# Kernel tuning notes

Measured on AMD Instinct MI355X. Metric: run time of the kernel, lower is better.

## Reference

```python
import jax, jax.numpy as jnp
import numpy as np

N_NODES = 50000
IN_DIM = 256
LATENT = 128
HIDDEN = 2 * LATENT  # 256


def _xavier(key, fan_in, fan_out):
    # matches nn.init.xavier_uniform_ on a [out, in] weight; we store as [in, out]
    limit = float(np.sqrt(6.0 / (fan_in + fan_out)))
    return jax.random.uniform(key, (fan_in, fan_out), jnp.float32, -limit, limit)


def setup_inputs() -> dict:
    key = jax.random.key(0)
    ks = jax.random.split(key, 8)
    x = jax.random.normal(ks[0], (N_NODES, IN_DIM), jnp.float32)
    edge_index = jax.random.randint(ks[1], (2, 800000), 0, N_NODES, jnp.int64)
    W1 = _xavier(ks[2], IN_DIM, HIDDEN)
    b1 = jnp.zeros((HIDDEN,), jnp.float32)
    Wmu = _xavier(ks[3], HIDDEN, LATENT)
    bmu = jnp.zeros((LATENT,), jnp.float32)
    Wlv = _xavier(ks[4], HIDDEN, LATENT)
    blv = jnp.zeros((LATENT,), jnp.float32)
    return {"x": x, "edge_index": edge_index, "W1": W1, "b1": b1,
            "Wmu": Wmu, "bmu": bmu, "Wlv": Wlv, "blv": blv}


def _gcn_layer(x, W, b, src, dst):
    # PyG GCNConv: h = x @ W; add self loops; symmetric norm; scatter-add; + bias
    h = x @ W  # [N, out]
    ones = jnp.ones(src.shape[0], x.dtype)
    deg = jax.ops.segment_sum(ones, dst, num_segments=N_NODES) + 1.0  # +1 for self loop
    dinv = jax.lax.rsqrt(deg)  # deg >= 1 always
    norm = dinv[src] * dinv[dst]  # [E]
    agg = jax.ops.segment_sum(h[src] * norm[:, None], dst, num_segments=N_NODES)
    agg = agg + h * (dinv * dinv)[:, None]  # self-loop contribution, norm_ii = 1/deg_i
    return agg + b


def reference(x, edge_index, W1, b1, Wmu, bmu, Wlv, blv):
    src, dst = edge_index[0], edge_index[1]
    z = _gcn_layer(x, W1, b1, src, dst)
    z = jax.nn.relu(z)
    # dropout in eval mode == identity
    mu = _gcn_layer(z, Wmu, bmu, src, dst)
    logvar = _gcn_layer(z, Wlv, blv, src, dst)
    return (mu, logvar)
```

## Files before the change

kernel.cpp:

```cpp
#include <hip/hip_runtime.h>

#define N_NODES 50000
#define E_EDGES 800000
#define D 256
#define L 128
#define CAP 64

typedef __attribute__((ext_vector_type(8))) short bf16x8;
typedef __attribute__((ext_vector_type(4))) float f32x4;

__device__ __forceinline__ float bf2f(unsigned short u) {
    union { unsigned int i; float f; } v; v.i = ((unsigned int)u) << 16; return v.f;
}
__device__ __forceinline__ unsigned short f2bf(float f) {
    union { float f; unsigned int i; } v; v.f = f;
    unsigned int r = v.i + 0x7fffu + ((v.i >> 16) & 1u);
    return (unsigned short)(r >> 16);
}

__global__ __launch_bounds__(256) void zero_i(int* __restrict__ p, int n) {
    int i = blockIdx.x * 256 + threadIdx.x;
    if (i < n) p[i] = 0;
}

__global__ __launch_bounds__(256) void fill_fixed(const int* __restrict__ src,
                                                  const int* __restrict__ dst,
                                                  int* __restrict__ cursor,
                                                  int* __restrict__ bucket) {
    int e = blockIdx.x * 256 + threadIdx.x;
    if (e >= E_EDGES) return;
    int d = dst[e];
    int pos = atomicAdd(&cursor[d], 1);
    if (pos < CAP) bucket[d * CAP + pos] = src[e];
}

__global__ __launch_bounds__(256) void dinv_fin(const int* __restrict__ cursor,
                                                float* __restrict__ dinv) {
    int i = blockIdx.x * 256 + threadIdx.x;
    if (i < N_NODES) dinv[i] = rsqrtf((float)cursor[i] + 1.0f);
}

__global__ __launch_bounds__(256) void prep_w(
    const float* __restrict__ W1, const float* __restrict__ Wmu,
    const float* __restrict__ Wlv, const float* __restrict__ bmu,
    const float* __restrict__ blv,
    unsigned short* __restrict__ W1h, unsigned short* __restrict__ W1l,
    unsigned short* __restrict__ Wch, unsigned short* __restrict__ Wcl,
    float* __restrict__ bcat) {
    int b = blockIdx.x, t = threadIdx.x;
    if (b < 256) {
        int n = b, k = t;
        float w = W1[k * 256 + n];
        unsigned short h = f2bf(w);
        W1h[n * 256 + k] = h;
        W1l[n * 256 + k] = f2bf(w - bf2f(h));
    } else {
        int n = b - 256, k = t;
        float w = (n < 128) ? Wmu[k * 128 + n] : Wlv[k * 128 + (n - 128)];
        unsigned short h = f2bf(w);
        Wch[n * 256 + k] = h;
        Wcl[n * 256 + k] = f2bf(w - bf2f(h));
        if (b == 256) bcat[t] = (t < 128) ? bmu[t] : blv[t - 128];
    }
}

__global__ __launch_bounds__(256, 3) void gemm_mfma(
    const float* __restrict__ A,
    const unsigned short* __restrict__ Bth, const unsigned short* __restrict__ Btl,
    unsigned short* __restrict__ Hout, int M)
{
    __shared__ unsigned short Bsh[256 * 32];
    __shared__ unsigned short Bsl[256 * 32];
    const int t = threadIdx.x;
    const int lane = t & 63, wave = t >> 6;
    const int row0 = blockIdx.x * 64 + wave * 16;
    const int m_ = lane & 15, q = lane >> 4;
    int rA = row0 + m_; if (rA >= M) rA = M - 1;
    const float* Ap = A + (size_t)rA * 256;
    const int bn = t >> 2;
    const int bc = t & 3;

    f32x4 acc[16];
    const f32x4 zf = {0.f, 0.f, 0.f, 0.f};
#pragma unroll
    for (int nt = 0; nt < 16; ++nt) acc[nt] = zf;

    for (int ks = 0; ks < 8; ++ks) {
        const int k0 = ks * 32;
        bf16x8 gbh[4], gbl[4];
#pragma unroll
        for (int i = 0; i < 4; ++i) {
            int n = bn + i * 64;
            gbh[i] = *(const bf16x8*)(Bth + n * 256 + k0 + bc * 8);
            gbl[i] = *(const bf16x8*)(Btl + n * 256 + k0 + bc * 8);
        }
        float4 av0 = *(const float4*)(Ap + k0 + q * 8);
        float4 av1 = *(const float4*)(Ap + k0 + q * 8 + 4);
        __syncthreads();
#pragma unroll
        for (int i = 0; i < 4; ++i) {
            int n = bn + i * 64;
            int cc = (bc ^ ((n >> 1) & 3)) * 8;
            *(bf16x8*)&Bsh[n * 32 + cc] = gbh[i];
            *(bf16x8*)&Bsl[n * 32 + cc] = gbl[i];
        }
        float af[8] = {av0.x, av0.y, av0.z, av0.w, av1.x, av1.y, av1.z, av1.w};
        bf16x8 ah, al;
#pragma unroll
        for (int j = 0; j < 8; ++j) {
            unsigned short h = f2bf(af[j]);
            ah[j] = (short)h;
            al[j] = (short)f2bf(af[j] - bf2f(h));
        }
        __syncthreads();
#pragma unroll
        for (int nt = 0; nt < 16; ++nt) {
            int n = nt * 16 + m_;
            int cr = (q ^ ((n >> 1) & 3)) * 8;
            bf16x8 bh = *(const bf16x8*)&Bsh[n * 32 + cr];
            bf16x8 bl = *(const bf16x8*)&Bsl[n * 32 + cr];
            acc[nt] = __builtin_amdgcn_mfma_f32_16x16x32_bf16(ah, bh, acc[nt], 0, 0, 0);
            acc[nt] = __builtin_amdgcn_mfma_f32_16x16x32_bf16(ah, bl, acc[nt], 0, 0, 0);
            acc[nt] = __builtin_amdgcn_mfma_f32_16x16x32_bf16(al, bh, acc[nt], 0, 0, 0);
        }
    }
    int rbase = row0 + q * 4;
#pragma unroll
    for (int r = 0; r < 4; ++r) {
        int grow = rbase + r;
        if (grow >= M) continue;
#pragma unroll
        for (int nt = 0; nt < 16; ++nt) {
            int gcol = nt * 16 + m_;
            Hout[(size_t)grow * 256 + gcol] = f2bf(acc[nt][r]);
        }
    }
}

__global__ __launch_bounds__(256, 3) void gemm_bf16(
    const unsigned short* __restrict__ A,
    const unsigned short* __restrict__ Bth, const unsigned short* __restrict__ Btl,
    unsigned short* __restrict__ Tout, int M)
{
    __shared__ unsigned short Bsh[256 * 32];
    __shared__ unsigned short Bsl[256 * 32];
    const int t = threadIdx.x;
    const int lane = t & 63, wave = t >> 6;
    const int row0 = blockIdx.x * 64 + wave * 16;
    const int m_ = lane & 15, q = lane >> 4;
    int rA = row0 + m_; if (rA >= M) rA = M - 1;
    const unsigned short* Ap = A + (size_t)rA * 256;
    const int bn = t >> 2;
    const int bc = t & 3;

    f32x4 acc[16];
    const f32x4 zf = {0.f, 0.f, 0.f, 0.f};
#pragma unroll
    for (int nt = 0; nt < 16; ++nt) acc[nt] = zf;

    for (int ks = 0; ks < 8; ++ks) {
        const int k0 = ks * 32;
        bf16x8 gbh[4], gbl[4];
#pragma unroll
        for (int i = 0; i < 4; ++i) {
            int n = bn + i * 64;
            gbh[i] = *(const bf16x8*)(Bth + n * 256 + k0 + bc * 8);
            gbl[i] = *(const bf16x8*)(Btl + n * 256 + k0 + bc * 8);
        }
        bf16x8 ah = *(const bf16x8*)(Ap + k0 + q * 8);
        __syncthreads();
#pragma unroll
        for (int i = 0; i < 4; ++i) {
            int n = bn + i * 64;
            int cc = (bc ^ ((n >> 1) & 3)) * 8;
            *(bf16x8*)&Bsh[n * 32 + cc] = gbh[i];
            *(bf16x8*)&Bsl[n * 32 + cc] = gbl[i];
        }
        __syncthreads();
#pragma unroll
        for (int nt = 0; nt < 16; ++nt) {
            int n = nt * 16 + m_;
            int cr = (q ^ ((n >> 1) & 3)) * 8;
            bf16x8 bh = *(const bf16x8*)&Bsh[n * 32 + cr];
            bf16x8 bl = *(const bf16x8*)&Bsl[n * 32 + cr];
            acc[nt] = __builtin_amdgcn_mfma_f32_16x16x32_bf16(ah, bh, acc[nt], 0, 0, 0);
            acc[nt] = __builtin_amdgcn_mfma_f32_16x16x32_bf16(ah, bl, acc[nt], 0, 0, 0);
        }
    }
    int rbase = row0 + q * 4;
#pragma unroll
    for (int r = 0; r < 4; ++r) {
        int grow = rbase + r;
        if (grow >= M) continue;
#pragma unroll
        for (int nt = 0; nt < 16; ++nt) {
            int gcol = nt * 16 + m_;
            Tout[(size_t)grow * 256 + gcol] = f2bf(acc[nt][r]);
        }
    }
}

__global__ __launch_bounds__(256) void gather_pre(
    const unsigned short* __restrict__ Hs,
    const int* __restrict__ bucket, const int* __restrict__ cnt_,
    const float* __restrict__ dinv, const float* __restrict__ bias,
    unsigned short* __restrict__ OutZ,
    float* __restrict__ mu, float* __restrict__ lv, int mode)
{
    const int lane = threadIdx.x & 63;
    const int hl = lane & 31;
    const int bb = lane & 32;
    const int node = blockIdx.x * 8 + (threadIdx.x >> 5);
    const int col = hl * 8;
    int cnt = cnt_[node]; if (cnt > CAP) cnt = CAP;
    float dn = dinv[node];

    int   s0r = 0, s1r = 0;
    float w0r = 0.f, w1r = 0.f;
    if (hl < cnt)      { s0r = bucket[node * CAP + hl];      w0r = dinv[s0r] * dn; }
    if (hl + 32 < cnt) { s1r = bucket[node * CAP + 32 + hl]; w1r = dinv[s1r] * dn; }

    float sl = dn * dn;
    bf16x8 hv = *(const bf16x8*)(Hs + (size_t)node * D + col);
    float a[8];
#pragma unroll
    for (int p = 0; p < 8; ++p) a[p] = bf2f((unsigned short)hv[p]) * sl;

    const int cnt0 = cnt < 32 ? cnt : 32;
    int j = 0;
    for (; j + 3 < cnt0; j += 4) {
        int t0 = __shfl(s0r, bb + j,     64), t1 = __shfl(s0r, bb + j + 1, 64);
        int t2 = __shfl(s0r, bb + j + 2, 64), t3 = __shfl(s0r, bb + j + 3, 64);
        float w0 = __shfl(w0r, bb + j,     64), w1 = __shfl(w0r, bb + j + 1, 64);
        float w2 = __shfl(w0r, bb + j + 2, 64), w3 = __shfl(w0r, bb + j + 3, 64);
        bf16x8 u0 = *(const bf16x8*)(Hs + (size_t)t0 * D + col);
        bf16x8 u1 = *(const bf16x8*)(Hs + (size_t)t1 * D + col);
        bf16x8 u2 = *(const bf16x8*)(Hs + (size_t)t2 * D + col);
        bf16x8 u3 = *(const bf16x8*)(Hs + (size_t)t3 * D + col);
#pragma unroll
        for (int p = 0; p < 8; ++p) a[p] = fmaf(bf2f((unsigned short)u0[p]), w0, a[p]);
#pragma unroll
        for (int p = 0; p < 8; ++p) a[p] = fmaf(bf2f((unsigned short)u1[p]), w1, a[p]);
#pragma unroll
        for (int p = 0; p < 8; ++p) a[p] = fmaf(bf2f((unsigned short)u2[p]), w2, a[p]);
#pragma unroll
        for (int p = 0; p < 8; ++p) a[p] = fmaf(bf2f((unsigned short)u3[p]), w3, a[p]);
    }
    for (; j < cnt0; ++j) {
        int   t0 = __shfl(s0r, bb + j, 64);
        float w0 = __shfl(w0r, bb + j, 64);
        bf16x8 u0 = *(const bf16x8*)(Hs + (size_t)t0 * D + col);
#pragma unroll
        for (int p = 0; p < 8; ++p) a[p] = fmaf(bf2f((unsigned short)u0[p]), w0, a[p]);
    }
    if (cnt > 32) {
        for (int j2 = 0; j2 < cnt - 32; ++j2) {
            int   t0 = __shfl(s1r, bb + j2, 64);
            float w0 = __shfl(w1r, bb + j2, 64);
            bf16x8 u0 = *(const bf16x8*)(Hs + (size_t)t0 * D + col);
#pragma unroll
            for (int p = 0; p < 8; ++p) a[p] = fmaf(bf2f((unsigned short)u0[p]), w0, a[p]);
        }
    }

    float4 b0 = *(const float4*)(bias + col);
    float4 b1 = *(const float4*)(bias + col + 4);
    float bf[8] = {b0.x, b0.y, b0.z, b0.w, b1.x, b1.y, b1.z, b1.w};
    if (mode == 0) {
        bf16x8 o;
#pragma unroll
        for (int p = 0; p < 8; ++p) o[p] = (short)f2bf(fmaxf(a[p] + bf[p], 0.f));
        *(bf16x8*)(OutZ + (size_t)node * D + col) = o;
    } else {
        float4 o0, o1;
        o0.x = a[0] + bf[0]; o0.y = a[1] + bf[1];
        o0.z = a[2] + bf[2]; o0.w = a[3] + bf[3];
        o1.x = a[4] + bf[4]; o1.y = a[5] + bf[5];
        o1.z = a[6] + bf[6]; o1.w = a[7] + bf[7];
        float* Op = (col < 128) ? (mu + (size_t)node * L + col)
                                : (lv + (size_t)node * L + (col - 128));
        *(float4*)Op = o0;
        *(float4*)(Op + 4) = o1;
    }
}

extern "C" void kernel_launch(void* const* d_in, const int* in_sizes, int n_in,
                              void* d_out, int out_size, void* d_ws, size_t ws_size,
                              hipStream_t stream) {
    const float* x   = (const float*)d_in[0];
    const int*   ei  = (const int*)d_in[1];
    const float* W1  = (const float*)d_in[2];
    const float* b1  = (const float*)d_in[3];
    const float* Wmu = (const float*)d_in[4];
    const float* bmu = (const float*)d_in[5];
    const float* Wlv = (const float*)d_in[6];
    const float* blv = (const float*)d_in[7];
    const int* src = ei;
    const int* dst = ei + E_EDGES;

    const size_t NF = (size_t)N_NODES * D;
    unsigned short* Hb = (unsigned short*)d_ws;
    unsigned short* Z  = Hb + NF;
    unsigned short* T  = Z + NF;
    unsigned short* W1h = T + NF;
    unsigned short* W1l = W1h + 65536;
    unsigned short* Wch = W1l + 65536;
    unsigned short* Wcl = Wch + 65536;
    float* bcat = (float*)(Wcl + 65536);
    float* dinv = bcat + 256;
    int* cursor = (int*)(dinv + N_NODES);
    int* bucket = cursor + N_NODES;
    float* mu = (float*)d_out;
    float* lv = mu + (size_t)N_NODES * L;

    zero_i<<<(N_NODES + 255) / 256, 256, 0, stream>>>(cursor, N_NODES);
    fill_fixed<<<(E_EDGES + 255) / 256, 256, 0, stream>>>(src, dst, cursor, bucket);
    dinv_fin<<<(N_NODES + 255) / 256, 256, 0, stream>>>(cursor, dinv);

    prep_w<<<512, 256, 0, stream>>>(W1, Wmu, Wlv, bmu, blv, W1h, W1l, Wch, Wcl, bcat);

    const int gemm_blocks = (N_NODES + 63) / 64;
    const int gat_blocks  = N_NODES / 8;
    gemm_mfma<<<gemm_blocks, 256, 0, stream>>>(x, W1h, W1l, Hb, N_NODES);
    gather_pre<<<gat_blocks, 256, 0, stream>>>(Hb, bucket, cursor, dinv, b1,
                                               Z, nullptr, nullptr, 0);
    gemm_bf16<<<gemm_blocks, 256, 0, stream>>>(Z, Wch, Wcl, T, N_NODES);
    gather_pre<<<gat_blocks, 256, 0, stream>>>(T, bucket, cursor, dinv, bcat,
                                               nullptr, mu, lv, 1);
}
```

Before: 336.2 us.

## Retile GEMMs to 128-row blocks with 2x2 wave grid and shared A tiles

Both dense GEMM kernels move from 64-row blocks, where each wave owns 16 rows and all 256 columns, to 128-row blocks split over a 2x2 grid of waves (64 rows by 128 columns each). A is staged through swizzled LDS, and each wave reuses every B fragment across four row subtiles. This cuts LDS traffic for B per MFMA and halves the number of blocks, at the cost of more accumulator registers and a lower occupancy bound (2 blocks per CU instead of 3). The cursor zeroing is also folded into the weight-prep kernel, removing one launch.

```diff
diff --git a/kernel.cpp b/kernel.cpp
--- a/kernel.cpp
+++ b/kernel.cpp
@@ -16,11 +16,6 @@
     union { float f; unsigned int i; } v; v.f = f;
     unsigned int r = v.i + 0x7fffu + ((v.i >> 16) & 1u);
     return (unsigned short)(r >> 16);
-}
-
-__global__ __launch_bounds__(256) void zero_i(int* __restrict__ p, int n) {
-    int i = blockIdx.x * 256 + threadIdx.x;
-    if (i < n) p[i] = 0;
 }
 
 __global__ __launch_bounds__(256) void fill_fixed(const int* __restrict__ src,
@@ -40,13 +35,13 @@
     if (i < N_NODES) dinv[i] = rsqrtf((float)cursor[i] + 1.0f);
 }
 
-__global__ __launch_bounds__(256) void prep_w(
+__global__ __launch_bounds__(256) void setup(
     const float* __restrict__ W1, const float* __restrict__ Wmu,
     const float* __restrict__ Wlv, const float* __restrict__ bmu,
     const float* __restrict__ blv,
     unsigned short* __restrict__ W1h, unsigned short* __restrict__ W1l,
     unsigned short* __restrict__ Wch, unsigned short* __restrict__ Wcl,
-    float* __restrict__ bcat) {
+    float* __restrict__ bcat, int* __restrict__ cursor) {
     int b = blockIdx.x, t = threadIdx.x;
     if (b < 256) {
         int n = b, k = t;
@@ -54,148 +49,208 @@
         unsigned short h = f2bf(w);
         W1h[n * 256 + k] = h;
         W1l[n * 256 + k] = f2bf(w - bf2f(h));
-    } else {
+    } else if (b < 512) {
         int n = b - 256, k = t;
         float w = (n < 128) ? Wmu[k * 128 + n] : Wlv[k * 128 + (n - 128)];
         unsigned short h = f2bf(w);
         Wch[n * 256 + k] = h;
         Wcl[n * 256 + k] = f2bf(w - bf2f(h));
         if (b == 256) bcat[t] = (t < 128) ? bmu[t] : blv[t - 128];
-    }
-}
-
-__global__ __launch_bounds__(256, 3) void gemm_mfma(
+    } else {
+        int i = (b - 512) * 256 + t;
+        if (i < N_NODES) cursor[i] = 0;
+    }
+}
+
+__global__ __launch_bounds__(256, 2) void gemm_mfma(
     const float* __restrict__ A,
     const unsigned short* __restrict__ Bth, const unsigned short* __restrict__ Btl,
     unsigned short* __restrict__ Hout, int M)
 {
+    __shared__ unsigned short Ash[128 * 32];
+    __shared__ unsigned short Asl[128 * 32];
     __shared__ unsigned short Bsh[256 * 32];
     __shared__ unsigned short Bsl[256 * 32];
     const int t = threadIdx.x;
     const int lane = t & 63, wave = t >> 6;
-    const int row0 = blockIdx.x * 64 + wave * 16;
     const int m_ = lane & 15, q = lane >> 4;
-    int rA = row0 + m_; if (rA >= M) rA = M - 1;
-    const float* Ap = A + (size_t)rA * 256;
-    const int bn = t >> 2;
-    const int bc = t & 3;
-
-    f32x4 acc[16];
+    const int wr = wave >> 1, wc = wave & 1;
+    const int row0 = blockIdx.x * 128;
+    const int sr = t >> 2;
+    const int sc = t & 3;
+
+    f32x4 acc[4][8];
     const f32x4 zf = {0.f, 0.f, 0.f, 0.f};
 #pragma unroll
-    for (int nt = 0; nt < 16; ++nt) acc[nt] = zf;
+    for (int rs = 0; rs < 4; ++rs)
+#pragma unroll
+        for (int nt = 0; nt < 8; ++nt) acc[rs][nt] = zf;
 
     for (int ks = 0; ks < 8; ++ks) {
         const int k0 = ks * 32;
         bf16x8 gbh[4], gbl[4];
 #pragma unroll
         for (int i = 0; i < 4; ++i) {
-            int n = bn + i * 64;
-            gbh[i] = *(const bf16x8*)(Bth + n * 256 + k0 + bc * 8);
-            gbl[i] = *(const bf16x8*)(Btl + n * 256 + k0 + bc * 8);
-        }
-        float4 av0 = *(const float4*)(Ap + k0 + q * 8);
-        float4 av1 = *(const float4*)(Ap + k0 + q * 8 + 4);
+            int n = sr + i * 64;
+            gbh[i] = *(const bf16x8*)(Bth + n * 256 + k0 + sc * 8);
+            gbl[i] = *(const bf16x8*)(Btl + n * 256 + k0 + sc * 8);
+        }
+        float4 ga0[2], ga1[2];
+#pragma unroll
+        for (int p = 0; p < 2; ++p) {
+            int r = row0 + p * 64 + sr; if (r >= M) r = M - 1;
+            const float* Xp = A + (size_t)r * 256 + k0 + sc * 8;
+            ga0[p] = *(const float4*)Xp;
+            ga1[p] = *(const float4*)(Xp + 4);
+        }
         __syncthreads();
 #pragma unroll
+        for (int p = 0; p < 2; ++p) {
+            int lr = p * 64 + sr;
+            int cc = (sc ^ ((lr >> 1) & 3)) * 8;
+            float af[8] = {ga0[p].x, ga0[p].y, ga0[p].z, ga0[p].w,
+                           ga1[p].x, ga1[p].y, ga1[p].z, ga1[p].w};
+            bf16x8 h, l;
+#pragma unroll
+            for (int j = 0; j < 8; ++j) {
+                unsigned short hh = f2bf(af[j]);
+                h[j] = (short)hh;
+                l[j] = (short)f2bf(af[j] - bf2f(hh));
+            }
+            *(bf16x8*)&Ash[lr * 32 + cc] = h;
+            *(bf16x8*)&Asl[lr * 32 + cc] = l;
+        }
+#pragma unroll
         for (int i = 0; i < 4; ++i) {
-            int n = bn + i * 64;
-            int cc = (bc ^ ((n >> 1) & 3)) * 8;
+            int n = sr + i * 64;
+            int cc = (sc ^ ((n >> 1) & 3)) * 8;
             *(bf16x8*)&Bsh[n * 32 + cc] = gbh[i];
             *(bf16x8*)&Bsl[n * 32 + cc] = gbl[i];
         }
-        float af[8] = {av0.x, av0.y, av0.z, av0.w, av1.x, av1.y, av1.z, av1.w};
-        bf16x8 ah, al;
-#pragma unroll
-        for (int j = 0; j < 8; ++j) {
-            unsigned short h = f2bf(af[j]);
-            ah[j] = (short)h;
-            al[j] = (short)f2bf(af[j] - bf2f(h));
-        }
         __syncthreads();
-#pragma unroll
-        for (int nt = 0; nt < 16; ++nt) {
-            int n = nt * 16 + m_;
+        bf16x8 ah[4], al[4];
+#pragma unroll
+        for (int rs = 0; rs < 4; ++rs) {
+            int r = wr * 64 + rs * 16 + m_;
+            int cc = (q ^ ((r >> 1) & 3)) * 8;
+            ah[rs] = *(const bf16x8*)&Ash[r * 32 + cc];
+            al[rs] = *(const bf16x8*)&Asl[r * 32 + cc];
+        }
+#pragma unroll
+        for (int nt = 0; nt < 8; ++nt) {
+            int n = wc * 128 + nt * 16 + m_;
             int cr = (q ^ ((n >> 1) & 3)) * 8;
             bf16x8 bh = *(const bf16x8*)&Bsh[n * 32 + cr];
             bf16x8 bl = *(const bf16x8*)&Bsl[n * 32 + cr];
-            acc[nt] = __builtin_amdgcn_mfma_f32_16x16x32_bf16(ah, bh, acc[nt], 0, 0, 0);
-            acc[nt] = __builtin_amdgcn_mfma_f32_16x16x32_bf16(ah, bl, acc[nt], 0, 0, 0);
-            acc[nt] = __builtin_amdgcn_mfma_f32_16x16x32_bf16(al, bh, acc[nt], 0, 0, 0);
-        }
-    }
-    int rbase = row0 + q * 4;
-#pragma unroll
-    for (int r = 0; r < 4; ++r) {
-        int grow = rbase + r;
-        if (grow >= M) continue;
-#pragma unroll
-        for (int nt = 0; nt < 16; ++nt) {
-            int gcol = nt * 16 + m_;
-            Hout[(size_t)grow * 256 + gcol] = f2bf(acc[nt][r]);
-        }
-    }
-}
-
-__global__ __launch_bounds__(256, 3) void gemm_bf16(
+#pragma unroll
+            for (int rs = 0; rs < 4; ++rs) {
+                acc[rs][nt] = __builtin_amdgcn_mfma_f32_16x16x32_bf16(ah[rs], bh, acc[rs][nt], 0, 0, 0);
+                acc[rs][nt] = __builtin_amdgcn_mfma_f32_16x16x32_bf16(ah[rs], bl, acc[rs][nt], 0, 0, 0);
+                acc[rs][nt] = __builtin_amdgcn_mfma_f32_16x16x32_bf16(al[rs], bh, acc[rs][nt], 0, 0, 0);
+            }
+        }
+    }
+#pragma unroll
+    for (int rs = 0; rs < 4; ++rs) {
+        int rbase = row0 + wr * 64 + rs * 16 + q * 4;
+#pragma unroll
+        for (int rr = 0; rr < 4; ++rr) {
+            int grow = rbase + rr;
+            if (grow >= M) continue;
+#pragma unroll
+            for (int nt = 0; nt < 8; ++nt) {
+                int gcol = wc * 128 + nt * 16 + m_;
+                Hout[(size_t)grow * 256 + gcol] = f2bf(acc[rs][nt][rr]);
+            }
+        }
+    }
+}
+
+__global__ __launch_bounds__(256, 2) void gemm_bf16(
     const unsigned short* __restrict__ A,
     const unsigned short* __restrict__ Bth, const unsigned short* __restrict__ Btl,
     unsigned short* __restrict__ Tout, int M)
 {
+    __shared__ unsigned short Ash[128 * 32];
     __shared__ unsigned short Bsh[256 * 32];
     __shared__ unsigned short Bsl[256 * 32];
     const int t = threadIdx.x;
     const int lane = t & 63, wave = t >> 6;
-    const int row0 = blockIdx.x * 64 + wave * 16;
     const int m_ = lane & 15, q = lane >> 4;
-    int rA = row0 + m_; if (rA >= M) rA = M - 1;
-    const unsigned short* Ap = A + (size_t)rA * 256;
-    const int bn = t >> 2;
-    const int bc = t & 3;
-
-    f32x4 acc[16];
+    const int wr = wave >> 1, wc = wave & 1;
+    const int row0 = blockIdx.x * 128;
+    const int sr = t >> 2;
+    const int sc = t & 3;
+
+    f32x4 acc[4][8];
     const f32x4 zf = {0.f, 0.f, 0.f, 0.f};
 #pragma unroll
-    for (int nt = 0; nt < 16; ++nt) acc[nt] = zf;
+    for (int rs = 0; rs < 4; ++rs)
+#pragma unroll
+        for (int nt = 0; nt < 8; ++nt) acc[rs][nt] = zf;
 
     for (int ks = 0; ks < 8; ++ks) {
         const int k0 = ks * 32;
         bf16x8 gbh[4], gbl[4];
 #pragma unroll
         for (int i = 0; i < 4; ++i) {
-            int n = bn + i * 64;
-            gbh[i] = *(const bf16x8*)(Bth + n * 256 + k0 + bc * 8);
-            gbl[i] = *(const bf16x8*)(Btl + n * 256 + k0 + bc * 8);
-        }
-        bf16x8 ah = *(const bf16x8*)(Ap + k0 + q * 8);
+            int n = sr + i * 64;
+            gbh[i] = *(const bf16x8*)(Bth + n * 256 + k0 + sc * 8);
+            gbl[i] = *(const bf16x8*)(Btl + n * 256 + k0 + sc * 8);
+        }
+        bf16x8 gav[2];
+#pragma unroll
+        for (int p = 0; p < 2; ++p) {
+            int r = row0 + p * 64 + sr; if (r >= M) r = M - 1;
+            gav[p] = *(const bf16x8*)(A + (size_t)r * 256 + k0 + sc * 8);
+        }
         __syncthreads();
 #pragma unroll
+        for (int p = 0; p < 2; ++p) {
+            int lr = p * 64 + sr;
+            int cc = (sc ^ ((lr >> 1) & 3)) * 8;
+            *(bf16x8*)&Ash[lr * 32 + cc] = gav[p];
+        }
+#pragma unroll
         for (int i = 0; i < 4; ++i) {
-            int n = bn + i * 64;
-            int cc = (bc ^ ((n >> 1) & 3)) * 8;
+            int n = sr + i * 64;
+            int cc = (sc ^ ((n >> 1) & 3)) * 8;
             *(bf16x8*)&Bsh[n * 32 + cc] = gbh[i];
             *(bf16x8*)&Bsl[n * 32 + cc] = gbl[i];
         }
         __syncthreads();
-#pragma unroll
-        for (int nt = 0; nt < 16; ++nt) {
-            int n = nt * 16 + m_;
+        bf16x8 ah[4];
+#pragma unroll
+        for (int rs = 0; rs < 4; ++rs) {
+            int r = wr * 64 + rs * 16 + m_;
+            int cc = (q ^ ((r >> 1) & 3)) * 8;
+            ah[rs] = *(const bf16x8*)&Ash[r * 32 + cc];
+        }
+#pragma unroll
+        for (int nt = 0; nt < 8; ++nt) {
+            int n = wc * 128 + nt * 16 + m_;
             int cr = (q ^ ((n >> 1) & 3)) * 8;
             bf16x8 bh = *(const bf16x8*)&Bsh[n * 32 + cr];
             bf16x8 bl = *(const bf16x8*)&Bsl[n * 32 + cr];
-            acc[nt] = __builtin_amdgcn_mfma_f32_16x16x32_bf16(ah, bh, acc[nt], 0, 0, 0);
-            acc[nt] = __builtin_amdgcn_mfma_f32_16x16x32_bf16(ah, bl, acc[nt], 0, 0, 0);
-        }
-    }
-    int rbase = row0 + q * 4;
-#pragma unroll
-    for (int r = 0; r < 4; ++r) {
-        int grow = rbase + r;
-        if (grow >= M) continue;
-#pragma unroll
-        for (int nt = 0; nt < 16; ++nt) {
-            int gcol = nt * 16 + m_;
-            Tout[(size_t)grow * 256 + gcol] = f2bf(acc[nt][r]);
+#pragma unroll
+            for (int rs = 0; rs < 4; ++rs) {
+                acc[rs][nt] = __builtin_amdgcn_mfma_f32_16x16x32_bf16(ah[rs], bh, acc[rs][nt], 0, 0, 0);
+                acc[rs][nt] = __builtin_amdgcn_mfma_f32_16x16x32_bf16(ah[rs], bl, acc[rs][nt], 0, 0, 0);
+            }
+        }
+    }
+#pragma unroll
+    for (int rs = 0; rs < 4; ++rs) {
+        int rbase = row0 + wr * 64 + rs * 16 + q * 4;
+#pragma unroll
+        for (int rr = 0; rr < 4; ++rr) {
+            int grow = rbase + rr;
+            if (grow >= M) continue;
+#pragma unroll
+            for (int nt = 0; nt < 8; ++nt) {
+                int gcol = wc * 128 + nt * 16 + m_;
+                Tout[(size_t)grow * 256 + gcol] = f2bf(acc[rs][nt][rr]);
+            }
         }
     }
 }
@@ -313,13 +368,12 @@
     float* mu = (float*)d_out;
     float* lv = mu + (size_t)N_NODES * L;
 
-    zero_i<<<(N_NODES + 255) / 256, 256, 0, stream>>>(cursor, N_NODES);
+    setup<<<512 + (N_NODES + 255) / 256, 256, 0, stream>>>(
+        W1, Wmu, Wlv, bmu, blv, W1h, W1l, Wch, Wcl, bcat, cursor);
     fill_fixed<<<(E_EDGES + 255) / 256, 256, 0, stream>>>(src, dst, cursor, bucket);
     dinv_fin<<<(N_NODES + 255) / 256, 256, 0, stream>>>(cursor, dinv);
 
-    prep_w<<<512, 256, 0, stream>>>(W1, Wmu, Wlv, bmu, blv, W1h, W1l, Wch, Wcl, bcat);
-
-    const int gemm_blocks = (N_NODES + 63) / 64;
+    const int gemm_blocks = (N_NODES + 127) / 128;
     const int gat_blocks  = N_NODES / 8;
     gemm_mfma<<<gemm_blocks, 256, 0, stream>>>(x, W1h, W1l, Hb, N_NODES);
     gather_pre<<<gat_blocks, 256, 0, stream>>>(Hb, bucket, cursor, dinv, b1,
```

Measured after the change: 315.2 us. 6.2% less time.
